# Kernel tuning notes

Measured on AMD Instinct MI355X. Metric: run time of the kernel, lower is better.

The kernel has to match this reference:

```python
import jax, jax.numpy as jnp
import numpy as np
from jax import lax

B = 1024          # batch
R = 100           # number of radical heads (TOP_RADICALS)


def _conv(x, w, b, padding):
    y = lax.conv_general_dilated(
        x, w, window_strides=(1, 1), padding=padding,
        dimension_numbers=('NCHW', 'OIHW', 'NCHW'))
    return y + b[None, :, None, None]


def _maxpool2(x):
    return lax.reduce_window(x, -jnp.inf, lax.max,
                             (1, 1, 2, 2), (1, 1, 2, 2), 'VALID')


def setup_inputs() -> dict:
    key = jax.random.key(0)
    ks = jax.random.split(key, 20)
    s = 0.05
    inp = {
        'x': jax.random.normal(ks[0], (B, 1, 98, 98), jnp.float32),
        'conv1_w': jax.random.normal(ks[1], (6, 1, 3, 3), jnp.float32) * s,
        'conv1_b': jnp.zeros((6,), jnp.float32),
        'conv2_w': jax.random.normal(ks[2], (4, 6, 6, 6), jnp.float32) * s,
        'conv2_b': jnp.zeros((4,), jnp.float32),
        'conv3_w': jax.random.normal(ks[3], (2, 4, 3, 3), jnp.float32) * s,
        'conv3_b': jnp.zeros((2,), jnp.float32),
        'fc1_w': jax.random.normal(ks[4], (200, 400), jnp.float32) * s,
        'fc1_b': jnp.zeros((400,), jnp.float32),
        'fc2_w': jax.random.normal(ks[5], (400, 200), jnp.float32) * s,
        'fc2_b': jnp.zeros((200,), jnp.float32),
        # all R per-radical heads stacked: Linear(200,140)->(140,84)->(84,42)->(42,4)
        'h1_w': jax.random.normal(ks[6], (R, 200, 140), jnp.float32) * s,
        'h1_b': jnp.zeros((R, 140), jnp.float32),
        'h2_w': jax.random.normal(ks[7], (R, 140, 84), jnp.float32) * s,
        'h2_b': jnp.zeros((R, 84), jnp.float32),
        'h3_w': jax.random.normal(ks[8], (R, 84, 42), jnp.float32) * s,
        'h3_b': jnp.zeros((R, 42), jnp.float32),
        'h4_w': jax.random.normal(ks[9], (R, 42, 4), jnp.float32) * s,
        'h4_b': jnp.zeros((R, 4), jnp.float32),
    }
    return inp


def reference(x, conv1_w, conv1_b, conv2_w, conv2_b, conv3_w, conv3_b,
              fc1_w, fc1_b, fc2_w, fc2_b,
              h1_w, h1_b, h2_w, h2_b, h3_w, h3_b, h4_w, h4_b):
    # conv trunk: conv -> relu -> maxpool, x3
    x = _maxpool2(jax.nn.relu(_conv(x, conv1_w, conv1_b, [(1, 1), (1, 1)])))  # [B,6,49,49]
    x = _maxpool2(jax.nn.relu(_conv(x, conv2_w, conv2_b, 'VALID')))           # [B,4,22,22]
    x = _maxpool2(jax.nn.relu(_conv(x, conv3_w, conv3_b, 'VALID')))           # [B,2,10,10]
    x = x.reshape(x.shape[0], -1)                                             # [B,200]
    # shared MLP trunk
    x = jax.nn.relu(x @ fc1_w + fc1_b)   # [B,400]
    x = jax.nn.relu(x @ fc2_w + fc2_b)   # [B,200]
    # R independent 4-layer heads, fused into batched einsums
    h = jax.nn.relu(jnp.einsum('bd,rdh->brh', x, h1_w) + h1_b)  # [B,R,140]
    h = jax.nn.relu(jnp.einsum('brd,rdh->brh', h, h2_w) + h2_b)  # [B,R,84]
    h = jax.nn.relu(jnp.einsum('brd,rdh->brh', h, h3_w) + h3_b)  # [B,R,42]
    h = jnp.einsum('brd,rdh->brh', h, h4_w) + h4_b               # [B,R,4]
    # torch.cat over heads along dim=1 == reshape [B, R*4]
    return h.reshape(h.shape[0], -1)
```

## Files before the change

### kernel.cpp

```cpp
#include <hip/hip_runtime.h>

#define NB 1024
#define NR 100

typedef _Float16 half_t;
typedef half_t f16x8 __attribute__((ext_vector_type(8)));
typedef float f32x4 __attribute__((ext_vector_type(4)));
typedef float f32x2 __attribute__((ext_vector_type(2)));

__device__ __forceinline__ int kmap2(int g, int j) {
    return g*4 + (j & 3) + ((j >> 2) << 4);
}

__device__ __forceinline__ f32x2 pkfma(f32x2 a, float s, f32x2 c) {
    return __builtin_elementwise_fma(a, (f32x2){s, s}, c);
}

#define GLDS(gsrc, ldst) \
    __builtin_amdgcn_global_load_lds( \
        (const __attribute__((address_space(1))) void*)(gsrc), \
        (__attribute__((address_space(3))) void*)(ldst), 16, 0, 0)

__global__ __launch_bounds__(256) void wpack_k(
        const float* __restrict__ c1w, const float* __restrict__ c2w,
        float* __restrict__ wp1, float* __restrict__ wp2) {
    const int t = threadIdx.x;
    if (t < 27) {
        const int k = t / 3, g = t - (t/3)*3;
        wp1[t*2+0] = c1w[(g*2+0)*9 + k];
        wp1[t*2+1] = c1w[(g*2+1)*9 + k];
    }
    for (int i = t; i < 432; i += 256) {
        const int ocg = i / 216, k = i - ocg*216;
        wp2[i*2+0] = c2w[(ocg*2+0)*216 + k];
        wp2[i*2+1] = c2w[(ocg*2+1)*216 + k];
    }
}

#define EOFF 2268
#define IO   1568
__global__ __launch_bounds__(256, 5) void conv12_k(const float* __restrict__ x,
        const float* __restrict__ wp1, const float* __restrict__ b1c,
        const float* __restrict__ wp2, const float* __restrict__ b2c,
        float* __restrict__ out) {
    __shared__ float img[3136];
    __shared__ float c1p[4374];
    const int blk = blockIdx.x;
    const int b  = blk >> 2;
    const int qy = (blk >> 1) & 1, qx = blk & 1;
    const int R0 = 44*qy - 1, C0 = 44*qx - 1;
    const int tid = threadIdx.x;
    const float* xb = x + (size_t)b * 9604;

    for (int i = tid; i < 3136; i += 256) {
        const int rr = i / 56, cc = i - rr*56;
        const int gr = R0 + rr, gc = C0 + cc;
        float v = 0.f;
        if (gr >= 0 && gr < 98 && gc >= 0 && gc < 98) v = xb[gr*98 + gc];
        img[((cc & 1) ? IO : 0) + rr*28 + (cc >> 1)] = v;
    }
    __syncthreads();

    for (int pos = tid; pos < 729; pos += 256) {
        const int py = pos / 27, px = pos - py*27;
        float p[4][4];
        #pragma unroll
        for (int u = 0; u < 4; ++u) {
            const int ro = (2*py + u)*28;
            p[u][0] = img[ro + px];
            p[u][2] = img[ro + px + 1];
            p[u][1] = img[IO + ro + px];
            p[u][3] = img[IO + ro + px + 1];
        }
        f32x2 a2[3][4];
        #pragma unroll
        for (int g = 0; g < 3; ++g) {
            const f32x2 bv = *(const f32x2*)(b1c + g*2);
            a2[g][0] = a2[g][1] = a2[g][2] = a2[g][3] = bv;
        }
        #pragma unroll
        for (int ky = 0; ky < 3; ++ky)
            #pragma unroll
            for (int kx = 0; kx < 3; ++kx) {
                const int k = ky*3 + kx;
                const float q0 = p[ky  ][kx], q1 = p[ky  ][kx+1];
                const float q2 = p[ky+1][kx], q3 = p[ky+1][kx+1];
                #pragma unroll
                for (int g = 0; g < 3; ++g) {
                    const f32x2 wv = *(const f32x2*)(wp1 + (k*3+g)*2);
                    a2[g][0] = pkfma(wv, q0, a2[g][0]);
                    a2[g][1] = pkfma(wv, q1, a2[g][1]);
                    a2[g][2] = pkfma(wv, q2, a2[g][2]);
                    a2[g][3] = pkfma(wv, q3, a2[g][3]);
                }
            }
        const int par = px & 1, pi = px >> 1;
        #pragma unroll
        for (int g = 0; g < 3; ++g) {
            const float m0 = fmaxf(fmaxf(a2[g][0].x, a2[g][1].x),
                                   fmaxf(a2[g][2].x, a2[g][3].x));
            const float m1 = fmaxf(fmaxf(a2[g][0].y, a2[g][1].y),
                                   fmaxf(a2[g][2].y, a2[g][3].y));
            const int e0 = par ? (EOFF + ((2*g    )*27 + py)*13 + pi)
                               : (((2*g    )*27 + py)*14 + pi);
            const int e1 = par ? (EOFF + ((2*g + 1)*27 + py)*13 + pi)
                               : (((2*g + 1)*27 + py)*14 + pi);
            c1p[e0] = fmaxf(m0, 0.f);
            c1p[e1] = fmaxf(m1, 0.f);
        }
    }
    __syncthreads();

    const int wv_ = tid >> 6;
    const int ich = __builtin_amdgcn_readfirstlane(tid >> 7);
    const int unit = ((wv_ & 1) << 6) | (tid & 63);
    const bool act = unit < 121;
    const int py = act ? unit / 11 : 0;
    const int px = act ? unit - py*11 : 0;
    const int y0 = 2*py;

    f32x2 acc[2][2][2] = {};
    if (act) {
        #pragma unroll
        for (int ic3 = 0; ic3 < 3; ++ic3) {
            const int ic = ich*3 + ic3;
            const float* pe0 = c1p + (ic*27 + y0)*14 + px;
            const float* po0 = c1p + EOFF + (ic*27 + y0)*13 + px;
            #pragma unroll
            for (int u = 0; u < 7; ++u) {
                const float* pe = pe0 + u*14;
                const float* po = po0 + u*13;
                float pr[7];
                pr[0] = pe[0]; pr[2] = pe[1]; pr[4] = pe[2]; pr[6] = pe[3];
                pr[1] = po[0]; pr[3] = po[1]; pr[5] = po[2];
                #pragma unroll
                for (int dy = 0; dy < 2; ++dy) {
                    const int ky = u - dy;
                    if (ky < 0 || ky > 5) continue;
                    #pragma unroll
                    for (int kx = 0; kx < 6; ++kx) {
                        const f32x2 w0 =
                            *(const f32x2*)(wp2 + (ic*36 + ky*6 + kx)*2);
                        const f32x2 w1 =
                            *(const f32x2*)(wp2 + 432 + (ic*36 + ky*6 + kx)*2);
                        acc[0][dy][0] = pkfma(w0, pr[0+kx], acc[0][dy][0]);
                        acc[0][dy][1] = pkfma(w0, pr[1+kx], acc[0][dy][1]);
                        acc[1][dy][0] = pkfma(w1, pr[0+kx], acc[1][dy][0]);
                        acc[1][dy][1] = pkfma(w1, pr[1+kx], acc[1][dy][1]);
                    }
                }
            }
        }
    }
    float* pbuf = img;
    if (act && ich == 1) {
        #pragma unroll
        for (int p = 0; p < 2; ++p)
            #pragma unroll
            for (int dy = 0; dy < 2; ++dy)
                #pragma unroll
                for (int dx = 0; dx < 2; ++dx) {
                    const int j = ((p*2 + dy)*2 + dx)*2;
                    pbuf[(j    )*128 + unit] = acc[p][dy][dx].x;
                    pbuf[(j + 1)*128 + unit] = acc[p][dy][dx].y;
                }
    }
    __syncthreads();
    if (act && ich == 0) {
        #pragma unroll
        for (int p = 0; p < 2; ++p)
            #pragma unroll
            for (int dy = 0; dy < 2; ++dy)
                #pragma unroll
                for (int dx = 0; dx < 2; ++dx) {
                    const int j = ((p*2 + dy)*2 + dx)*2;
                    acc[p][dy][dx].x += pbuf[(j    )*128 + unit];
                    acc[p][dy][dx].y += pbuf[(j + 1)*128 + unit];
                }
        const int PY = qy*11 + py, PX = qx*11 + px;
        #pragma unroll
        for (int p = 0; p < 2; ++p) {
            const f32x2 bv = *(const f32x2*)(b2c + p*2);
            const float m0 = fmaxf(fmaxf(acc[p][0][0].x, acc[p][0][1].x),
                                   fmaxf(acc[p][1][0].x, acc[p][1][1].x)) + bv.x;
            const float m1 = fmaxf(fmaxf(acc[p][0][0].y, acc[p][0][1].y),
                                   fmaxf(acc[p][1][0].y, acc[p][1][1].y)) + bv.y;
            out[(((size_t)b*4 + p*2    )*22 + PY)*22 + PX] = fmaxf(m0, 0.f);
            out[(((size_t)b*4 + p*2 + 1)*22 + PY)*22 + PX] = fmaxf(m1, 0.f);
        }
    }
}

__global__ __launch_bounds__(256) void conv3_k(const float* __restrict__ in,
        const float* __restrict__ w, const float* __restrict__ bias,
        float* __restrict__ out) {
    __shared__ float sm[1936];
    const int b = blockIdx.x;
    const int tid = threadIdx.x;
    const float* src = in + (size_t)b * 1936;
    for (int i = tid; i < 484; i += 256)
        ((float4*)sm)[i] = ((const float4*)src)[i];
    __syncthreads();
    if (tid < 200) {
        const int c = tid / 100;
        const int rem = tid % 100;
        const int py = rem / 10, px = rem % 10;
        const int y0 = 2*py, x0 = 2*px;
        float a0, a1, a2, a3;
        a0 = a1 = a2 = a3 = bias[c];
        #pragma unroll
        for (int ic = 0; ic < 4; ++ic) {
            float p[4][4];
            const float* base = sm + ic*484 + y0*22 + x0;
            #pragma unroll
            for (int u = 0; u < 4; ++u)
                #pragma unroll
                for (int v = 0; v < 4; ++v)
                    p[u][v] = base[u*22 + v];
            #pragma unroll
            for (int ky = 0; ky < 3; ++ky) {
                #pragma unroll
                for (int kx = 0; kx < 3; ++kx) {
                    const float wv = w[(c*4 + ic)*9 + ky*3 + kx];
                    a0 = fmaf(wv, p[ky  ][kx  ], a0);
                    a1 = fmaf(wv, p[ky  ][kx+1], a1);
                    a2 = fmaf(wv, p[ky+1][kx  ], a2);
                    a3 = fmaf(wv, p[ky+1][kx+1], a3);
                }
            }
        }
        float m = fmaxf(fmaxf(a0, a1), fmaxf(a2, a3));
        out[(size_t)b*200 + tid] = fmaxf(m, 0.f);
    }
}

template<bool G0OUT>
__device__ __forceinline__ void gemm_body(float* pool, int bx, int by,
        const float* __restrict__ A, int lda,
        const float* __restrict__ W, const float* __restrict__ bias,
        float* __restrict__ C, int ldc,
        int M, int N, int K,
        half_t* __restrict__ g0h, half_t* __restrict__ g0l) {
    float (*As)[132] = (float(*)[132])pool;
    float* Ws = pool + 32*132;
    const int m0 = by * 128;
    const int n0 = bx * 64;
    const int tid = threadIdx.x;
    const int ti = tid >> 4, tj = tid & 15;
    float acc[8][4];
    #pragma unroll
    for (int i = 0; i < 8; ++i)
        #pragma unroll
        for (int j = 0; j < 4; ++j) acc[i][j] = 0.f;

    for (int k0 = 0; k0 < K; k0 += 32) {
        #pragma unroll
        for (int i = 0; i < 4; ++i) {
            const int f = tid + i*256;
            const int m = f >> 3, kg = f & 7;
            const int kk = kg*4;
            float4 v = make_float4(0.f, 0.f, 0.f, 0.f);
            if (k0 + kk < K)
                v = *(const float4*)(A + (long)(m0 + m)*lda + k0 + kk);
            As[kk+0][m] = v.x;
            As[kk+1][m] = v.y;
            As[kk+2][m] = v.z;
            As[kk+3][m] = v.w;
        }
        #pragma unroll
        for (int i = 0; i < 2; ++i) {
            const int f = tid + i*256;
            const int kk = f >> 4, cg = f & 15;
            const int n = n0 + cg*4;
            float4 v = make_float4(0.f, 0.f, 0.f, 0.f);
            if (k0 + kk < K) {
                const float* wp = W + (long)(k0 + kk)*N;
                if (n + 3 < N) v = *(const float4*)(wp + n);
                else {
                    if (n+0 < N) v.x = wp[n+0];
                    if (n+1 < N) v.y = wp[n+1];
                    if (n+2 < N) v.z = wp[n+2];
                }
            }
            *(float4*)&Ws[kk*64 + cg*4] = v;
        }
        __syncthreads();
        #pragma unroll
        for (int kk = 0; kk < 32; ++kk) {
            float a[8], wv[4];
            *(float4*)&a[0] = *(const float4*)&As[kk][ti*8];
            *(float4*)&a[4] = *(const float4*)&As[kk][ti*8 + 4];
            *(float4*)&wv[0] = *(const float4*)&Ws[kk*64 + tj*4];
            #pragma unroll
            for (int i = 0; i < 8; ++i)
                #pragma unroll
                for (int j = 0; j < 4; ++j)
                    acc[i][j] = fmaf(a[i], wv[j], acc[i][j]);
        }
        __syncthreads();
    }

    const int nb = n0 + tj*4;
    float bv[4] = {0.f, 0.f, 0.f, 0.f};
    #pragma unroll
    for (int e = 0; e < 4; ++e) if (nb + e < N) bv[e] = bias[nb + e];

    if (!G0OUT) {
        #pragma unroll
        for (int i = 0; i < 8; ++i) {
            const long m = m0 + ti*8 + i;
            if (nb + 3 < N) {
                float4 v;
                v.x = fmaxf(acc[i][0] + bv[0], 0.f);
                v.y = fmaxf(acc[i][1] + bv[1], 0.f);
                v.z = fmaxf(acc[i][2] + bv[2], 0.f);
                v.w = fmaxf(acc[i][3] + bv[3], 0.f);
                *(float4*)(C + m*(long)ldc + nb) = v;
            } else {
                #pragma unroll
                for (int j = 0; j < 4; ++j)
                    if (nb + j < N)
                        C[m*(long)ldc + nb + j] = fmaxf(acc[i][j] + bv[j], 0.f);
            }
        }
    } else {
        #pragma unroll
        for (int i = 0; i < 8; ++i) {
            const int m = m0 + ti*8 + i;
            #pragma unroll
            for (int j = 0; j < 4; ++j) {
                const int k = nb + j;
                if (k < 224) {
                    float v = 0.f;
                    if (k < N) v = fmaxf(acc[i][j] + bv[j], 0.f);
                    const half_t hi = (half_t)v;
                    const half_t lo = (half_t)(v - (float)hi);
                    const int kc = k >> 5, klo = k & 31;
                    const int h = klo >> 4, rm = klo & 15;
                    const int gg = rm >> 2, rr = rm & 3;
                    const size_t idx =
                        ((size_t)((m >> 4)*7 + kc)*64 + (gg << 4) + (m & 15))*8
                        + h*4 + rr;
                    g0h[idx] = hi;
                    g0l[idx] = lo;
                }
            }
        }
    }
}

__global__ __launch_bounds__(256, 4) void fc1_k(
        const float* __restrict__ A, const float* __restrict__ W,
        const float* __restrict__ bias, float* __restrict__ C) {
    __shared__ float pool[32*132 + 32*64];
    gemm_body<false>(pool, blockIdx.x, blockIdx.y, A, 200, W, bias, C, 400,
                     NB, 400, 200, nullptr, nullptr);
}

__global__ __launch_bounds__(256, 4) void fc2ws_k(
        const float* __restrict__ A, const float* __restrict__ W,
        const float* __restrict__ bias,
        half_t* __restrict__ g0h, half_t* __restrict__ g0l,
        const float* __restrict__ w1, const float* __restrict__ w2,
        const float* __restrict__ w3, const float* __restrict__ w4,
        half_t* __restrict__ f1h, half_t* __restrict__ f1l,
        half_t* __restrict__ f2h, half_t* __restrict__ f2l,
        half_t* __restrict__ f3h, half_t* __restrict__ f3l,
        half_t* __restrict__ f4h, half_t* __restrict__ f4l) {
    __shared__ float pool[32*132 + 32*64];
    const int bid = blockIdx.x;
    const int tid = threadIdx.x;
    if (bid < 32) {
        gemm_body<true>(pool, bid & 3, bid >> 2, A, 400, W, bias,
                        nullptr, 0, NB, 200, 400, g0h, g0l);
        return;
    }
    const int w = bid - 32;
    const int cx = w % 17, r = w / 17;
    float* lds = pool;
    int K, N, KC, NF, kc;
    const float* src;
    half_t *dh, *dl;
    if (cx < 7)       { K=200; N=140; KC=7; NF=9; kc=cx;    src=w1; dh=f1h; dl=f1l; }
    else if (cx < 12) { K=140; N=84;  KC=5; NF=6; kc=cx-7;  src=w2; dh=f2h; dl=f2l; }
    else if (cx < 15) { K=84;  N=42;  KC=3; NF=3; kc=cx-12; src=w3; dh=f3h; dl=f3l; }
    else              { K=42;  N=4;   KC=2; NF=1; kc=cx-15; src=w4; dh=f4h; dl=f4l; }
    const float* sb = src + (size_t)r * K * N;
    for (int i = tid; i < 32*N; i += 256) {
        const int kk = i / N, n = i - kk*N;
        const int kg = kc*32 + kk;
        lds[kk*N + n] = (kg < K) ? sb[(size_t)kg*N + n] : 0.f;
    }
    __syncthreads();
    const size_t base = ((size_t)r*KC + kc)*NF*512;
    for (int e = tid; e < NF*512; e += 256) {
        const int nf = e >> 9, rem = e & 511;
        const int l = rem >> 3, j = rem & 7;
        const int g = l >> 4, c = l & 15;
        const int kl = kmap2(g, j);
        const int n = nf*16 + c;
        const float v = (n < N) ? lds[kl*N + n] : 0.f;
        const half_t hi = (half_t)v;
        const half_t lo = (half_t)(v - (float)hi);
        dh[base + (size_t)nf*512 + rem] = hi;
        dl[base + (size_t)nf*512 + rem] = lo;
    }
}

#define MFMA(a, b, c) __builtin_amdgcn_mfma_f32_16x16x32_f16(a, b, c, 0, 0, 0)

__global__ __launch_bounds__(256, 2) void head_k(
        const half_t* __restrict__ g0h, const half_t* __restrict__ g0l,
        const half_t* __restrict__ w1h, const half_t* __restrict__ w1l,
        const half_t* __restrict__ w2h, const half_t* __restrict__ w2l,
        const half_t* __restrict__ w3h, const half_t* __restrict__ w3l,
        const half_t* __restrict__ w4h, const half_t* __restrict__ w4l,
        const float* __restrict__ b1, const float* __restrict__ b2,
        const float* __restrict__ b3, const float* __restrict__ b4,
        float* __restrict__ out) {
    constexpr int CH = 18*512;
    __shared__ half_t wb[2*CH];
    __shared__ float bl[270];
    const int bid = blockIdx.x;
    const int cx  = bid & 7;
    const int kb  = bid >> 3;
    const int r   = ((kb >> 3) << 3) + cx;
    if (r >= NR) return;
    const int mt  = kb & 7;
    const int tid = threadIdx.x;
    if (tid < 140) bl[tid]       = b1[(size_t)r*140 + tid];
    if (tid < 84)  bl[140 + tid] = b2[(size_t)r*84  + tid];
    if (tid < 42)  bl[224 + tid] = b3[(size_t)r*42  + tid];
    if (tid < 4)   bl[266 + tid] = b4[(size_t)r*4   + tid];
    const int w = tid >> 6, l = tid & 63;
    const int g4 = ((l >> 4) & 3) * 4;
    const int mb0 = mt*8 + w*2;
    const size_t loff = (size_t)l * 8;

    auto stage1 = [&](int kc, half_t* buf) {
        const half_t* hs = w1h + ((size_t)r*7 + kc)*9*512;
        const half_t* ls = w1l + ((size_t)r*7 + kc)*9*512;
        #pragma unroll
        for (int p0 = 0; p0 < 3; ++p0) {
            const int p = w + p0*4;
            if (p < 9) {
                GLDS(hs + (size_t)p*512 + loff, buf + p*512);
                GLDS(ls + (size_t)p*512 + loff, buf + (9+p)*512);
            }
        }
    };
    auto stage2 = [&](int kc, half_t* buf) {
        const half_t* hs = w2h + ((size_t)r*5 + kc)*6*512;
        const half_t* ls = w2l + ((size_t)r*5 + kc)*6*512;
        #pragma unroll
        for (int p0 = 0; p0 < 2; ++p0) {
            const int p = w + p0*4;
            if (p < 6) {
                GLDS(hs + (size_t)p*512 + loff, buf + p*512);
                GLDS(ls + (size_t)p*512 + loff, buf + (6+p)*512);
            }
        }
    };
    auto stage3 = [&](int kc, half_t* buf) {
        const half_t* hs = w3h + ((size_t)r*3 + kc)*3*512;
        const half_t* ls = w3l + ((size_t)r*3 + kc)*3*512;
        if (w < 3) {
            GLDS(hs + (size_t)w*512 + loff, buf + w*512);
            GLDS(ls + (size_t)w*512 + loff, buf + (3+w)*512);
        }
    };

    f16x8 bhv[2][2], blv[2][2];
    stage1(0, wb);
    #pragma unroll
    for (int mb = 0; mb < 2; ++mb) {
        const size_t bo = ((size_t)(mb0 + mb)*7 + 0)*512 + loff;
        bhv[0][mb] = *(const f16x8*)(g0h + bo);
        blv[0][mb] = *(const f16x8*)(g0l + bo);
    }
    __syncthreads();
    f32x4 a1[2][9] = {};
    #pragma unroll
    for (int kc = 0; kc < 7; ++kc) {
        const half_t* cur = wb + (kc & 1)*CH;
        if (kc < 6) {
            stage1(kc+1, wb + ((kc+1) & 1)*CH);
            #pragma unroll
            for (int mb = 0; mb < 2; ++mb) {
                const size_t bo = ((size_t)(mb0 + mb)*7 + kc + 1)*512 + loff;
                bhv[(kc+1)&1][mb] = *(const f16x8*)(g0h + bo);
                blv[(kc+1)&1][mb] = *(const f16x8*)(g0l + bo);
            }
        } else {
            stage2(0, wb + CH);
        }
        #pragma unroll
        for (int nf = 0; nf < 9; ++nf) {
            const f16x8 wh = *(const f16x8*)(cur + nf*512 + loff);
            const f16x8 wl = *(const f16x8*)(cur + (9+nf)*512 + loff);
            #pragma unroll
            for (int mb = 0; mb < 2; ++mb) {
                a1[mb][nf] = MFMA(wh, bhv[kc&1][mb], a1[mb][nf]);
                a1[mb][nf] = MFMA(wh, blv[kc&1][mb], a1[mb][nf]);
                a1[mb][nf] = MFMA(wl, bhv[kc&1][mb], a1[mb][nf]);
            }
        }
        __syncthreads();
    }
    f16x8 b2h[2][5], b2l[2][5];
    #pragma unroll
    for (int kc = 0; kc < 5; ++kc)
        #pragma unroll
        for (int h = 0; h < 2; ++h) {
            const int nf = kc*2 + h;
            #pragma unroll
            for (int mb = 0; mb < 2; ++mb)
                #pragma unroll
                for (int rr = 0; rr < 4; ++rr) {
                    float v = 0.f;
                    if (nf < 9) {
                        const int n = nf*16 + g4 + rr;
                        v = (n < 140) ? fmaxf(a1[mb][nf][rr] + bl[n], 0.f) : 0.f;
                    }
                    const half_t hi = (half_t)v;
                    const half_t lo = (half_t)(v - (float)hi);
                    b2h[mb][kc][h*4+rr] = hi;
                    b2l[mb][kc][h*4+rr] = lo;
                }
        }
    f32x4 a2[2][6] = {};
    #pragma unroll
    for (int kc = 0; kc < 5; ++kc) {
        const half_t* cur = wb + (((kc+1) & 1))*CH;
        if (kc < 4) stage2(kc+1, wb + (kc & 1)*CH);
        else        stage3(0,    wb + (kc & 1)*CH);
        #pragma unroll
        for (int nf = 0; nf < 6; ++nf) {
            const f16x8 wh = *(const f16x8*)(cur + nf*512 + loff);
            const f16x8 wl = *(const f16x8*)(cur + (6+nf)*512 + loff);
            #pragma unroll
            for (int mb = 0; mb < 2; ++mb) {
                a2[mb][nf] = MFMA(wh, b2h[mb][kc], a2[mb][nf]);
                a2[mb][nf] = MFMA(wh, b2l[mb][kc], a2[mb][nf]);
                a2[mb][nf] = MFMA(wl, b2h[mb][kc], a2[mb][nf]);
            }
        }
        __syncthreads();
    }
    f16x8 b3h[2][3], b3l[2][3];
    #pragma unroll
    for (int kc = 0; kc < 3; ++kc)
        #pragma unroll
        for (int h = 0; h < 2; ++h) {
            const int nf = kc*2 + h;
            #pragma unroll
            for (int mb = 0; mb < 2; ++mb)
                #pragma unroll
                for (int rr = 0; rr < 4; ++rr) {
                    float v = 0.f;
                    if (nf < 6) {
                        const int n = nf*16 + g4 + rr;
                        v = (n < 84) ? fmaxf(a2[mb][nf][rr] + bl[140 + n], 0.f) : 0.f;
                    }
                    const half_t hi = (half_t)v;
                    const half_t lo = (half_t)(v - (float)hi);
                    b3h[mb][kc][h*4+rr] = hi;
                    b3l[mb][kc][h*4+rr] = lo;
                }
        }
    f32x4 a3[2][3] = {};
    #pragma unroll
    for (int kc = 0; kc < 3; ++kc) {
        const half_t* cur = wb + (kc & 1)*CH;
        if (kc < 2) stage3(kc+1, wb + ((kc+1) & 1)*CH);
        #pragma unroll
        for (int nf = 0; nf < 3; ++nf) {
            const f16x8 wh = *(const f16x8*)(cur + nf*512 + loff);
            const f16x8 wl = *(const f16x8*)(cur + (3+nf)*512 + loff);
            #pragma unroll
            for (int mb = 0; mb < 2; ++mb) {
                a3[mb][nf] = MFMA(wh, b3h[mb][kc], a3[mb][nf]);
                a3[mb][nf] = MFMA(wh, b3l[mb][kc], a3[mb][nf]);
                a3[mb][nf] = MFMA(wl, b3h[mb][kc], a3[mb][nf]);
            }
        }
        __syncthreads();
    }
    f16x8 b4h[2][2], b4l[2][2];
    #pragma unroll
    for (int kc = 0; kc < 2; ++kc)
        #pragma unroll
        for (int h = 0; h < 2; ++h) {
            const int nf = kc*2 + h;
            #pragma unroll
            for (int mb = 0; mb < 2; ++mb)
                #pragma unroll
                for (int rr = 0; rr < 4; ++rr) {
                    float v = 0.f;
                    if (nf < 3) {
                        const int n = nf*16 + g4 + rr;
                        v = (n < 42) ? fmaxf(a3[mb][nf][rr] + bl[224 + n], 0.f) : 0.f;
                    }
                    const half_t hi = (half_t)v;
                    const half_t lo = (half_t)(v - (float)hi);
                    b4h[mb][kc][h*4+rr] = hi;
                    b4l[mb][kc][h*4+rr] = lo;
                }
        }
    f32x4 a4[2] = {};
    #pragma unroll
    for (int kc = 0; kc < 2; ++kc) {
        const size_t wo = ((size_t)r*2 + kc)*512 + loff;
        const f16x8 wh = *(const f16x8*)(w4h + wo);
        const f16x8 wl = *(const f16x8*)(w4l + wo);
        #pragma unroll
        for (int mb = 0; mb < 2; ++mb) {
            a4[mb] = MFMA(wh, b4h[mb][kc], a4[mb]);
            a4[mb] = MFMA(wh, b4l[mb][kc], a4[mb]);
            a4[mb] = MFMA(wl, b4h[mb][kc], a4[mb]);
        }
    }
    if ((l >> 4) == 0) {
        #pragma unroll
        for (int mb = 0; mb < 2; ++mb) {
            const int b = (mb0 + mb)*16 + (l & 15);
            float4 o;
            o.x = a4[mb][0] + bl[266];
            o.y = a4[mb][1] + bl[267];
            o.z = a4[mb][2] + bl[268];
            o.w = a4[mb][3] + bl[269];
            *(float4*)(out + (size_t)b*400 + r*4) = o;
        }
    }
}

extern "C" void kernel_launch(void* const* d_in, const int* in_sizes, int n_in,
                              void* d_out, int out_size, void* d_ws, size_t ws_size,
                              hipStream_t stream) {
    const float* x    = (const float*)d_in[0];
    const float* c1w  = (const float*)d_in[1];
    const float* c1b  = (const float*)d_in[2];
    const float* c2w  = (const float*)d_in[3];
    const float* c2b  = (const float*)d_in[4];
    const float* c3w  = (const float*)d_in[5];
    const float* c3b  = (const float*)d_in[6];
    const float* fc1w = (const float*)d_in[7];
    const float* fc1b = (const float*)d_in[8];
    const float* fc2w = (const float*)d_in[9];
    const float* fc2b = (const float*)d_in[10];
    const float* h1w  = (const float*)d_in[11];
    const float* h1b  = (const float*)d_in[12];
    const float* h2w  = (const float*)d_in[13];
    const float* h2b  = (const float*)d_in[14];
    const float* h3w  = (const float*)d_in[15];
    const float* h3b  = (const float*)d_in[16];
    const float* h4w  = (const float*)d_in[17];
    const float* h4b  = (const float*)d_in[18];
    float* out = (float*)d_out;

    char* ws = (char*)d_ws;
    size_t o = 0;
    float* t2 = (float*)(ws + o); o += (size_t)NB*4*484*4;
    float* t3 = (float*)(ws + o); o += (size_t)NB*200*4;
    float* f1 = (float*)(ws + o); o += (size_t)NB*400*4;
    half_t* g0h = (half_t*)(ws + o); o += (size_t)64*7*512*2;
    half_t* g0l = (half_t*)(ws + o); o += (size_t)64*7*512*2;
    half_t* w1h = (half_t*)(ws + o); o += (size_t)NR*7*9*512*2;
    half_t* w1l = (half_t*)(ws + o); o += (size_t)NR*7*9*512*2;
    half_t* w2h = (half_t*)(ws + o); o += (size_t)NR*5*6*512*2;
    half_t* w2l = (half_t*)(ws + o); o += (size_t)NR*5*6*512*2;
    half_t* w3h = (half_t*)(ws + o); o += (size_t)NR*3*3*512*2;
    half_t* w3l = (half_t*)(ws + o); o += (size_t)NR*3*3*512*2;
    half_t* w4h = (half_t*)(ws + o); o += (size_t)NR*2*1*512*2;
    half_t* w4l = (half_t*)(ws + o); o += (size_t)NR*2*1*512*2;
    float* wp1 = (float*)(ws + o); o += 64*4;
    float* wp2 = (float*)(ws + o); o += 896*4;

    wpack_k<<<1, 256, 0, stream>>>(c1w, c2w, wp1, wp2);
    conv12_k<<<NB*4, 256, 0, stream>>>(x, wp1, c1b, wp2, c2b, t2);
    conv3_k<<<NB, 256, 0, stream>>>(t2, c3w, c3b, t3);
    fc1_k<<<dim3(7, 8), 256, 0, stream>>>(t3, fc1w, fc1b, f1);
    fc2ws_k<<<32 + 1700, 256, 0, stream>>>(f1, fc2w, fc2b, g0h, g0l,
        h1w, h2w, h3w, h4w, w1h, w1l, w2h, w2l, w3h, w3l, w4h, w4l);
    head_k<<<832, 256, 0, stream>>>(
        g0h, g0l, w1h, w1l, w2h, w2l, w3h, w3l, w4h, w4l,
        h1b, h2b, h3b, h4b, out);

    (void)in_sizes; (void)n_in; (void)out_size; (void)ws_size;
}
```

Measured before the change: 184.3 us.

## Move head weight packing into conv kernel, drop wpack, halve head tile per wave

The head-weight fp16 hi/lo packing blocks move out of the fc2 kernel and are appended to the conv1/2 grid. There they can overlap with the large conv work, and fc2 becomes a small 32-block GEMM. The separate conv weight-pack kernel is removed, and conv weights are read directly from their original layout as scalar loads. The head kernel now gives each wave one 16-row batch tile instead of two and doubles the grid, trading weight reuse for more blocks and higher occupancy (launch bounds 4).

```diff
diff --git a/kernel.cpp b/kernel.cpp
--- a/kernel.cpp
+++ b/kernel.cpp
@@ -21,35 +21,61 @@
         (const __attribute__((address_space(1))) void*)(gsrc), \
         (__attribute__((address_space(3))) void*)(ldst), 16, 0, 0)
 
-__global__ __launch_bounds__(256) void wpack_k(
-        const float* __restrict__ c1w, const float* __restrict__ c2w,
-        float* __restrict__ wp1, float* __restrict__ wp2) {
-    const int t = threadIdx.x;
-    if (t < 27) {
-        const int k = t / 3, g = t - (t/3)*3;
-        wp1[t*2+0] = c1w[(g*2+0)*9 + k];
-        wp1[t*2+1] = c1w[(g*2+1)*9 + k];
-    }
-    for (int i = t; i < 432; i += 256) {
-        const int ocg = i / 216, k = i - ocg*216;
-        wp2[i*2+0] = c2w[(ocg*2+0)*216 + k];
-        wp2[i*2+1] = c2w[(ocg*2+1)*216 + k];
-    }
-}
-
 #define EOFF 2268
 #define IO   1568
-__global__ __launch_bounds__(256, 5) void conv12_k(const float* __restrict__ x,
-        const float* __restrict__ wp1, const float* __restrict__ b1c,
-        const float* __restrict__ wp2, const float* __restrict__ b2c,
-        float* __restrict__ out) {
-    __shared__ float img[3136];
-    __shared__ float c1p[4374];
-    const int blk = blockIdx.x;
-    const int b  = blk >> 2;
-    const int qy = (blk >> 1) & 1, qx = blk & 1;
+__global__ __launch_bounds__(256, 5) void conv12ws_k(const float* __restrict__ x,
+        const float* __restrict__ c1w, const float* __restrict__ b1c,
+        const float* __restrict__ c2w, const float* __restrict__ b2c,
+        float* __restrict__ out,
+        const float* __restrict__ w1, const float* __restrict__ w2,
+        const float* __restrict__ w3, const float* __restrict__ w4,
+        half_t* __restrict__ f1h, half_t* __restrict__ f1l,
+        half_t* __restrict__ f2h, half_t* __restrict__ f2l,
+        half_t* __restrict__ f3h, half_t* __restrict__ f3l,
+        half_t* __restrict__ f4h, half_t* __restrict__ f4l) {
+    __shared__ float pool[7510];
+    const int bid = blockIdx.x;
+    const int tid = threadIdx.x;
+
+    if (bid >= 4096) {
+        const int wq = bid - 4096;
+        const int cx = wq % 17, r = wq / 17;
+        float* lds = pool;
+        int K, N, KC, NF, kc;
+        const float* src;
+        half_t *dh, *dl;
+        if (cx < 7)       { K=200; N=140; KC=7; NF=9; kc=cx;    src=w1; dh=f1h; dl=f1l; }
+        else if (cx < 12) { K=140; N=84;  KC=5; NF=6; kc=cx-7;  src=w2; dh=f2h; dl=f2l; }
+        else if (cx < 15) { K=84;  N=42;  KC=3; NF=3; kc=cx-12; src=w3; dh=f3h; dl=f3l; }
+        else              { K=42;  N=4;   KC=2; NF=1; kc=cx-15; src=w4; dh=f4h; dl=f4l; }
+        const float* sb = src + (size_t)r * K * N;
+        for (int i = tid; i < 32*N; i += 256) {
+            const int kk = i / N, n = i - kk*N;
+            const int kg = kc*32 + kk;
+            lds[kk*N + n] = (kg < K) ? sb[(size_t)kg*N + n] : 0.f;
+        }
+        __syncthreads();
+        const size_t base = ((size_t)r*KC + kc)*NF*512;
+        for (int e = tid; e < NF*512; e += 256) {
+            const int nf = e >> 9, rem = e & 511;
+            const int l = rem >> 3, j = rem & 7;
+            const int g = l >> 4, c = l & 15;
+            const int kl = kmap2(g, j);
+            const int n = nf*16 + c;
+            const float v = (n < N) ? lds[kl*N + n] : 0.f;
+            const half_t hi = (half_t)v;
+            const half_t lo = (half_t)(v - (float)hi);
+            dh[base + (size_t)nf*512 + rem] = hi;
+            dl[base + (size_t)nf*512 + rem] = lo;
+        }
+        return;
+    }
+
+    float* img = pool;
+    float* c1p = pool + 3136;
+    const int b  = bid >> 2;
+    const int qy = (bid >> 1) & 1, qx = bid & 1;
     const int R0 = 44*qy - 1, C0 = 44*qx - 1;
-    const int tid = threadIdx.x;
     const float* xb = x + (size_t)b * 9604;
 
     for (int i = tid; i < 3136; i += 256) {
@@ -75,7 +101,7 @@
         f32x2 a2[3][4];
         #pragma unroll
         for (int g = 0; g < 3; ++g) {
-            const f32x2 bv = *(const f32x2*)(b1c + g*2);
+            const f32x2 bv = {b1c[g*2], b1c[g*2+1]};
             a2[g][0] = a2[g][1] = a2[g][2] = a2[g][3] = bv;
         }
         #pragma unroll
@@ -87,7 +113,7 @@
                 const float q2 = p[ky+1][kx], q3 = p[ky+1][kx+1];
                 #pragma unroll
                 for (int g = 0; g < 3; ++g) {
-                    const f32x2 wv = *(const f32x2*)(wp1 + (k*3+g)*2);
+                    const f32x2 wv = {c1w[(g*2)*9 + k], c1w[(g*2+1)*9 + k]};
                     a2[g][0] = pkfma(wv, q0, a2[g][0]);
                     a2[g][1] = pkfma(wv, q1, a2[g][1]);
                     a2[g][2] = pkfma(wv, q2, a2[g][2]);
@@ -139,10 +165,9 @@
                     if (ky < 0 || ky > 5) continue;
                     #pragma unroll
                     for (int kx = 0; kx < 6; ++kx) {
-                        const f32x2 w0 =
-                            *(const f32x2*)(wp2 + (ic*36 + ky*6 + kx)*2);
-                        const f32x2 w1 =
-                            *(const f32x2*)(wp2 + 432 + (ic*36 + ky*6 + kx)*2);
+                        const int idx = ic*36 + ky*6 + kx;
+                        const f32x2 w0 = {c2w[idx],       c2w[216 + idx]};
+                        const f32x2 w1 = {c2w[432 + idx], c2w[648 + idx]};
                         acc[0][dy][0] = pkfma(w0, pr[0+kx], acc[0][dy][0]);
                         acc[0][dy][1] = pkfma(w0, pr[1+kx], acc[0][dy][1]);
                         acc[1][dy][0] = pkfma(w1, pr[0+kx], acc[1][dy][0]);
@@ -180,11 +205,10 @@
         const int PY = qy*11 + py, PX = qx*11 + px;
         #pragma unroll
         for (int p = 0; p < 2; ++p) {
-            const f32x2 bv = *(const f32x2*)(b2c + p*2);
             const float m0 = fmaxf(fmaxf(acc[p][0][0].x, acc[p][0][1].x),
-                                   fmaxf(acc[p][1][0].x, acc[p][1][1].x)) + bv.x;
+                                   fmaxf(acc[p][1][0].x, acc[p][1][1].x)) + b2c[p*2];
             const float m1 = fmaxf(fmaxf(acc[p][0][0].y, acc[p][0][1].y),
-                                   fmaxf(acc[p][1][0].y, acc[p][1][1].y)) + bv.y;
+                                   fmaxf(acc[p][1][0].y, acc[p][1][1].y)) + b2c[p*2+1];
             out[(((size_t)b*4 + p*2    )*22 + PY)*22 + PX] = fmaxf(m0, 0.f);
             out[(((size_t)b*4 + p*2 + 1)*22 + PY)*22 + PX] = fmaxf(m1, 0.f);
         }
@@ -357,59 +381,18 @@
                      NB, 400, 200, nullptr, nullptr);
 }
 
-__global__ __launch_bounds__(256, 4) void fc2ws_k(
+__global__ __launch_bounds__(256, 4) void fc2_k(
         const float* __restrict__ A, const float* __restrict__ W,
         const float* __restrict__ bias,
-        half_t* __restrict__ g0h, half_t* __restrict__ g0l,
-        const float* __restrict__ w1, const float* __restrict__ w2,
-        const float* __restrict__ w3, const float* __restrict__ w4,
-        half_t* __restrict__ f1h, half_t* __restrict__ f1l,
-        half_t* __restrict__ f2h, half_t* __restrict__ f2l,
-        half_t* __restrict__ f3h, half_t* __restrict__ f3l,
-        half_t* __restrict__ f4h, half_t* __restrict__ f4l) {
+        half_t* __restrict__ g0h, half_t* __restrict__ g0l) {
     __shared__ float pool[32*132 + 32*64];
-    const int bid = blockIdx.x;
-    const int tid = threadIdx.x;
-    if (bid < 32) {
-        gemm_body<true>(pool, bid & 3, bid >> 2, A, 400, W, bias,
-                        nullptr, 0, NB, 200, 400, g0h, g0l);
-        return;
-    }
-    const int w = bid - 32;
-    const int cx = w % 17, r = w / 17;
-    float* lds = pool;
-    int K, N, KC, NF, kc;
-    const float* src;
-    half_t *dh, *dl;
-    if (cx < 7)       { K=200; N=140; KC=7; NF=9; kc=cx;    src=w1; dh=f1h; dl=f1l; }
-    else if (cx < 12) { K=140; N=84;  KC=5; NF=6; kc=cx-7;  src=w2; dh=f2h; dl=f2l; }
-    else if (cx < 15) { K=84;  N=42;  KC=3; NF=3; kc=cx-12; src=w3; dh=f3h; dl=f3l; }
-    else              { K=42;  N=4;   KC=2; NF=1; kc=cx-15; src=w4; dh=f4h; dl=f4l; }
-    const float* sb = src + (size_t)r * K * N;
-    for (int i = tid; i < 32*N; i += 256) {
-        const int kk = i / N, n = i - kk*N;
-        const int kg = kc*32 + kk;
-        lds[kk*N + n] = (kg < K) ? sb[(size_t)kg*N + n] : 0.f;
-    }
-    __syncthreads();
-    const size_t base = ((size_t)r*KC + kc)*NF*512;
-    for (int e = tid; e < NF*512; e += 256) {
-        const int nf = e >> 9, rem = e & 511;
-        const int l = rem >> 3, j = rem & 7;
-        const int g = l >> 4, c = l & 15;
-        const int kl = kmap2(g, j);
-        const int n = nf*16 + c;
-        const float v = (n < N) ? lds[kl*N + n] : 0.f;
-        const half_t hi = (half_t)v;
-        const half_t lo = (half_t)(v - (float)hi);
-        dh[base + (size_t)nf*512 + rem] = hi;
-        dl[base + (size_t)nf*512 + rem] = lo;
-    }
+    gemm_body<true>(pool, blockIdx.x & 3, blockIdx.x >> 2, A, 400, W, bias,
+                    nullptr, 0, NB, 200, 400, g0h, g0l);
 }
 
 #define MFMA(a, b, c) __builtin_amdgcn_mfma_f32_16x16x32_f16(a, b, c, 0, 0, 0)
 
-__global__ __launch_bounds__(256, 2) void head_k(
+__global__ __launch_bounds__(256, 4) void head_k(
         const half_t* __restrict__ g0h, const half_t* __restrict__ g0l,
         const half_t* __restrict__ w1h, const half_t* __restrict__ w1l,
         const half_t* __restrict__ w2h, const half_t* __restrict__ w2l,
@@ -423,10 +406,10 @@
     __shared__ float bl[270];
     const int bid = blockIdx.x;
     const int cx  = bid & 7;
-    const int kb  = bid >> 3;
-    const int r   = ((kb >> 3) << 3) + cx;
+    const int kq  = bid >> 3;
+    const int r   = ((kq >> 4) << 3) + cx;
     if (r >= NR) return;
-    const int mt  = kb & 7;
+    const int mt  = kq & 15;
     const int tid = threadIdx.x;
     if (tid < 140) bl[tid]       = b1[(size_t)r*140 + tid];
     if (tid < 84)  bl[140 + tid] = b2[(size_t)r*84  + tid];
@@ -434,7 +417,7 @@
     if (tid < 4)   bl[266 + tid] = b4[(size_t)r*4   + tid];
     const int w = tid >> 6, l = tid & 63;
     const int g4 = ((l >> 4) & 3) * 4;
-    const int mb0 = mt*8 + w*2;
+    const int mb0 = mt*4 + w;
     const size_t loff = (size_t)l * 8;
 
     auto stage1 = [&](int kc, half_t* buf) {
@@ -470,27 +453,23 @@
         }
     };
 
-    f16x8 bhv[2][2], blv[2][2];
+    f16x8 bhv[2], blv[2];
     stage1(0, wb);
-    #pragma unroll
-    for (int mb = 0; mb < 2; ++mb) {
-        const size_t bo = ((size_t)(mb0 + mb)*7 + 0)*512 + loff;
-        bhv[0][mb] = *(const f16x8*)(g0h + bo);
-        blv[0][mb] = *(const f16x8*)(g0l + bo);
+    {
+        const size_t bo = ((size_t)mb0*7 + 0)*512 + loff;
+        bhv[0] = *(const f16x8*)(g0h + bo);
+        blv[0] = *(const f16x8*)(g0l + bo);
     }
     __syncthreads();
-    f32x4 a1[2][9] = {};
+    f32x4 a1[9] = {};
     #pragma unroll
     for (int kc = 0; kc < 7; ++kc) {
         const half_t* cur = wb + (kc & 1)*CH;
         if (kc < 6) {
             stage1(kc+1, wb + ((kc+1) & 1)*CH);
-            #pragma unroll
-            for (int mb = 0; mb < 2; ++mb) {
-                const size_t bo = ((size_t)(mb0 + mb)*7 + kc + 1)*512 + loff;
-                bhv[(kc+1)&1][mb] = *(const f16x8*)(g0h + bo);
-                blv[(kc+1)&1][mb] = *(const f16x8*)(g0l + bo);
-            }
+            const size_t bo = ((size_t)mb0*7 + kc + 1)*512 + loff;
+            bhv[(kc+1)&1] = *(const f16x8*)(g0h + bo);
+            blv[(kc+1)&1] = *(const f16x8*)(g0l + bo);
         } else {
             stage2(0, wb + CH);
         }
@@ -498,37 +477,32 @@
         for (int nf = 0; nf < 9; ++nf) {
             const f16x8 wh = *(const f16x8*)(cur + nf*512 + loff);
             const f16x8 wl = *(const f16x8*)(cur + (9+nf)*512 + loff);
-            #pragma unroll
-            for (int mb = 0; mb < 2; ++mb) {
-                a1[mb][nf] = MFMA(wh, bhv[kc&1][mb], a1[mb][nf]);
-                a1[mb][nf] = MFMA(wh, blv[kc&1][mb], a1[mb][nf]);
-                a1[mb][nf] = MFMA(wl, bhv[kc&1][mb], a1[mb][nf]);
-            }
+            a1[nf] = MFMA(wh, bhv[kc&1], a1[nf]);
+            a1[nf] = MFMA(wh, blv[kc&1], a1[nf]);
+            a1[nf] = MFMA(wl, bhv[kc&1], a1[nf]);
         }
         __syncthreads();
     }
-    f16x8 b2h[2][5], b2l[2][5];
+    f16x8 b2h[5], b2l[5];
     #pragma unroll
     for (int kc = 0; kc < 5; ++kc)
         #pragma unroll
         for (int h = 0; h < 2; ++h) {
             const int nf = kc*2 + h;
             #pragma unroll
-            for (int mb = 0; mb < 2; ++mb)
-                #pragma unroll
-                for (int rr = 0; rr < 4; ++rr) {
-                    float v = 0.f;
-                    if (nf < 9) {
-                        const int n = nf*16 + g4 + rr;
-                        v = (n < 140) ? fmaxf(a1[mb][nf][rr] + bl[n], 0.f) : 0.f;
-                    }
-                    const half_t hi = (half_t)v;
-                    const half_t lo = (half_t)(v - (float)hi);
-                    b2h[mb][kc][h*4+rr] = hi;
-                    b2l[mb][kc][h*4+rr] = lo;
-                }
-        }
-    f32x4 a2[2][6] = {};
+            for (int rr = 0; rr < 4; ++rr) {
+                float v = 0.f;
+                if (nf < 9) {
+                    const int n = nf*16 + g4 + rr;
+                    v = (n < 140) ? fmaxf(a1[nf][rr] + bl[n], 0.f) : 0.f;
+                }
+                const half_t hi = (half_t)v;
+                const half_t lo = (half_t)(v - (float)hi);
+                b2h[kc][h*4+rr] = hi;
+                b2l[kc][h*4+rr] = lo;
+            }
+        }
+    f32x4 a2[6] = {};
     #pragma unroll
     for (int kc = 0; kc < 5; ++kc) {
         const half_t* cur = wb + (((kc+1) & 1))*CH;
@@ -538,37 +512,32 @@
         for (int nf = 0; nf < 6; ++nf) {
             const f16x8 wh = *(const f16x8*)(cur + nf*512 + loff);
             const f16x8 wl = *(const f16x8*)(cur + (6+nf)*512 + loff);
-            #pragma unroll
-            for (int mb = 0; mb < 2; ++mb) {
-                a2[mb][nf] = MFMA(wh, b2h[mb][kc], a2[mb][nf]);
-                a2[mb][nf] = MFMA(wh, b2l[mb][kc], a2[mb][nf]);
-                a2[mb][nf] = MFMA(wl, b2h[mb][kc], a2[mb][nf]);
-            }
+            a2[nf] = MFMA(wh, b2h[kc], a2[nf]);
+            a2[nf] = MFMA(wh, b2l[kc], a2[nf]);
+            a2[nf] = MFMA(wl, b2h[kc], a2[nf]);
         }
         __syncthreads();
     }
-    f16x8 b3h[2][3], b3l[2][3];
+    f16x8 b3h[3], b3l[3];
     #pragma unroll
     for (int kc = 0; kc < 3; ++kc)
         #pragma unroll
         for (int h = 0; h < 2; ++h) {
             const int nf = kc*2 + h;
             #pragma unroll
-            for (int mb = 0; mb < 2; ++mb)
-                #pragma unroll
-                for (int rr = 0; rr < 4; ++rr) {
-                    float v = 0.f;
-                    if (nf < 6) {
-                        const int n = nf*16 + g4 + rr;
-                        v = (n < 84) ? fmaxf(a2[mb][nf][rr] + bl[140 + n], 0.f) : 0.f;
-                    }
-                    const half_t hi = (half_t)v;
-                    const half_t lo = (half_t)(v - (float)hi);
-                    b3h[mb][kc][h*4+rr] = hi;
-                    b3l[mb][kc][h*4+rr] = lo;
-                }
-        }
-    f32x4 a3[2][3] = {};
+            for (int rr = 0; rr < 4; ++rr) {
+                float v = 0.f;
+                if (nf < 6) {
+                    const int n = nf*16 + g4 + rr;
+                    v = (n < 84) ? fmaxf(a2[nf][rr] + bl[140 + n], 0.f) : 0.f;
+                }
+                const half_t hi = (half_t)v;
+                const half_t lo = (half_t)(v - (float)hi);
+                b3h[kc][h*4+rr] = hi;
+                b3l[kc][h*4+rr] = lo;
+            }
+        }
+    f32x4 a3[3] = {};
     #pragma unroll
     for (int kc = 0; kc < 3; ++kc) {
         const half_t* cur = wb + (kc & 1)*CH;
@@ -577,60 +546,49 @@
         for (int nf = 0; nf < 3; ++nf) {
             const f16x8 wh = *(const f16x8*)(cur + nf*512 + loff);
             const f16x8 wl = *(const f16x8*)(cur + (3+nf)*512 + loff);
-            #pragma unroll
-            for (int mb = 0; mb < 2; ++mb) {
-                a3[mb][nf] = MFMA(wh, b3h[mb][kc], a3[mb][nf]);
-                a3[mb][nf] = MFMA(wh, b3l[mb][kc], a3[mb][nf]);
-                a3[mb][nf] = MFMA(wl, b3h[mb][kc], a3[mb][nf]);
-            }
+            a3[nf] = MFMA(wh, b3h[kc], a3[nf]);
+            a3[nf] = MFMA(wh, b3l[kc], a3[nf]);
+            a3[nf] = MFMA(wl, b3h[kc], a3[nf]);
         }
         __syncthreads();
     }
-    f16x8 b4h[2][2], b4l[2][2];
+    f16x8 b4h[2], b4l[2];
     #pragma unroll
     for (int kc = 0; kc < 2; ++kc)
         #pragma unroll
         for (int h = 0; h < 2; ++h) {
             const int nf = kc*2 + h;
             #pragma unroll
-            for (int mb = 0; mb < 2; ++mb)
-                #pragma unroll
-                for (int rr = 0; rr < 4; ++rr) {
-                    float v = 0.f;
-                    if (nf < 3) {
-                        const int n = nf*16 + g4 + rr;
-                        v = (n < 42) ? fmaxf(a3[mb][nf][rr] + bl[224 + n], 0.f) : 0.f;
-                    }
-                    const half_t hi = (half_t)v;
-                    const half_t lo = (half_t)(v - (float)hi);
-                    b4h[mb][kc][h*4+rr] = hi;
-                    b4l[mb][kc][h*4+rr] = lo;
-                }
-        }
-    f32x4 a4[2] = {};
+            for (int rr = 0; rr < 4; ++rr) {
+                float v = 0.f;
+                if (nf < 3) {
+                    const int n = nf*16 + g4 + rr;
+                    v = (n < 42) ? fmaxf(a3[nf][rr] + bl[224 + n], 0.f) : 0.f;
+                }
+                const half_t hi = (half_t)v;
+                const half_t lo = (half_t)(v - (float)hi);
+                b4h[kc][h*4+rr] = hi;
+                b4l[kc][h*4+rr] = lo;
+            }
+        }
+    f32x4 a4 = {};
     #pragma unroll
     for (int kc = 0; kc < 2; ++kc) {
         const size_t wo = ((size_t)r*2 + kc)*512 + loff;
         const f16x8 wh = *(const f16x8*)(w4h + wo);
         const f16x8 wl = *(const f16x8*)(w4l + wo);
-        #pragma unroll
-        for (int mb = 0; mb < 2; ++mb) {
-            a4[mb] = MFMA(wh, b4h[mb][kc], a4[mb]);
-            a4[mb] = MFMA(wh, b4l[mb][kc], a4[mb]);
-            a4[mb] = MFMA(wl, b4h[mb][kc], a4[mb]);
-        }
+        a4 = MFMA(wh, b4h[kc], a4);
+        a4 = MFMA(wh, b4l[kc], a4);
+        a4 = MFMA(wl, b4h[kc], a4);
     }
     if ((l >> 4) == 0) {
-        #pragma unroll
-        for (int mb = 0; mb < 2; ++mb) {
-            const int b = (mb0 + mb)*16 + (l & 15);
-            float4 o;
-            o.x = a4[mb][0] + bl[266];
-            o.y = a4[mb][1] + bl[267];
-            o.z = a4[mb][2] + bl[268];
-            o.w = a4[mb][3] + bl[269];
-            *(float4*)(out + (size_t)b*400 + r*4) = o;
-        }
+        const int b = mb0*16 + (l & 15);
+        float4 o;
+        o.x = a4[0] + bl[266];
+        o.y = a4[1] + bl[267];
+        o.z = a4[2] + bl[268];
+        o.w = a4[3] + bl[269];
+        *(float4*)(out + (size_t)b*400 + r*4) = o;
     }
 }
 
@@ -673,16 +631,13 @@
     half_t* w3l = (half_t*)(ws + o); o += (size_t)NR*3*3*512*2;
     half_t* w4h = (half_t*)(ws + o); o += (size_t)NR*2*1*512*2;
     half_t* w4l = (half_t*)(ws + o); o += (size_t)NR*2*1*512*2;
-    float* wp1 = (float*)(ws + o); o += 64*4;
-    float* wp2 = (float*)(ws + o); o += 896*4;
-
-    wpack_k<<<1, 256, 0, stream>>>(c1w, c2w, wp1, wp2);
-    conv12_k<<<NB*4, 256, 0, stream>>>(x, wp1, c1b, wp2, c2b, t2);
+
+    conv12ws_k<<<4096 + 1700, 256, 0, stream>>>(x, c1w, c1b, c2w, c2b, t2,
+        h1w, h2w, h3w, h4w, w1h, w1l, w2h, w2l, w3h, w3l, w4h, w4l);
     conv3_k<<<NB, 256, 0, stream>>>(t2, c3w, c3b, t3);
     fc1_k<<<dim3(7, 8), 256, 0, stream>>>(t3, fc1w, fc1b, f1);
-    fc2ws_k<<<32 + 1700, 256, 0, stream>>>(f1, fc2w, fc2b, g0h, g0l,
-        h1w, h2w, h3w, h4w, w1h, w1l, w2h, w2l, w3h, w3l, w4h, w4l);
-    head_k<<<832, 256, 0, stream>>>(
+    fc2_k<<<32, 256, 0, stream>>>(f1, fc2w, fc2b, g0h, g0l);
+    head_k<<<1664, 256, 0, stream>>>(
         g0h, g0l, w1h, w1l, w2h, w2l, w3h, w3l, w4h, w4l,
         h1b, h2b, h3b, h4b, out);
 
```

Measured after the change: 191.5 us. 1.04x slower.
